# Kernel optimization log

Hardware: AMD Instinct MI355X
Metric: run time of the kernel (lower is better)

## Reference

```python
import jax, jax.numpy as jnp
import numpy as np
from jax import lax

H, W = 480, 320
BS, PAD, SF, WIN = 20, 6, 4, 32        # block, zero-pad, scale, window = BS+2*PAD
NH, NW = H // BS, W // BS              # 24, 16 -> 384 blocks


def _conv(x, w, b, stride=1, pad=0):
    out = lax.conv_general_dilated(x, w, (stride, stride), [(pad, pad), (pad, pad)],
                                   dimension_numbers=('NCHW', 'OIHW', 'NCHW'))
    return out + b[None, :, None, None]


def _rep_conv(x, w, b):  # 3x3 conv with replicate padding (padding_mode='replicate')
    xp = jnp.pad(x, ((0, 0), (0, 0), (1, 1), (1, 1)), mode='edge')
    return _conv(xp, w, b)


def _maxpool2(x):
    return lax.reduce_window(x, -jnp.inf, lax.max, (1, 1, 2, 2), (1, 1, 2, 2), 'VALID')


def _pixel_shuffle(x, r=SF):  # (N, C*r*r, h, w) -> (N, C, h*r, w*r), torch ordering
    n, crr, h, w = x.shape
    c = crr // (r * r)
    return x.reshape(n, c, r, r, h, w).transpose(0, 1, 4, 2, 5, 3).reshape(n, c, h * r, w * r)


def _he(key, shape):
    std = np.sqrt(2.0 / (shape[0] * shape[2] * shape[3]))
    return jax.random.normal(key, shape, jnp.float32) * std


def setup_inputs() -> dict:
    key = jax.random.key(0)
    ks = jax.random.split(key, 16)
    return {
        'x': jax.random.normal(ks[0], (1, 3, H, W), jnp.float32),
        'cls_w1': _he(ks[1], (32, 3, 3, 3)),  'cls_b1': jnp.zeros((32,), jnp.float32),
        'cls_w2': _he(ks[2], (32, 32, 3, 3)), 'cls_b2': jnp.zeros((32,), jnp.float32),
        'cls_w3': _he(ks[3], (16, 32, 3, 3)), 'cls_b3': jnp.zeros((16,), jnp.float32),
        'cls_w4': _he(ks[4], (8, 16, 3, 3)),  'cls_b4': jnp.zeros((8,), jnp.float32),
        'cls_w5': _he(ks[5], (1, 8, 5, 5)),   'cls_b5': jnp.zeros((1,), jnp.float32),
        'lt_w1': _he(ks[6], (16, 3, 3, 3)),   'lt_b1': jnp.zeros((16,), jnp.float32),
        'lt_w2': _he(ks[7], (48, 16, 3, 3)),  'lt_b2': jnp.zeros((48,), jnp.float32),
        'cx_w1': _he(ks[8], (64, 3, 3, 3)),   'cx_b1': jnp.zeros((64,), jnp.float32),
        'cx_w2': _he(ks[9], (64, 64, 3, 3)),  'cx_b2': jnp.zeros((64,), jnp.float32),
        'cx_w3': _he(ks[10], (48, 64, 3, 3)), 'cx_b3': jnp.zeros((48,), jnp.float32),
    }


def reference(x, cls_w1, cls_b1, cls_w2, cls_b2, cls_w3, cls_b3, cls_w4, cls_b4,
              cls_w5, cls_b5, lt_w1, lt_b1, lt_w2, lt_b2,
              cx_w1, cx_b1, cx_w2, cx_b2, cx_w3, cx_b3):
    relu = jax.nn.relu
    # ---- classifier (gate) ----
    h = relu(_rep_conv(x, cls_w1, cls_b1))
    h = _maxpool2(relu(_rep_conv(h, cls_w2, cls_b2)))
    h = relu(_rep_conv(h, cls_w3, cls_b3))
    h = _maxpool2(relu(_rep_conv(h, cls_w4, cls_b4)))
    h = _conv(h, cls_w5, cls_b5, stride=BS // 4)          # (1,1,NH,NW)
    class_vector = jax.nn.sigmoid(h.reshape(-1))          # (NH*NW,)

    # ---- blockify (overlapping 32x32 windows, stride 20, zero pad 6) ----
    xp = jnp.pad(x, ((0, 0), (0, 0), (PAD, PAD), (PAD, PAD)))
    hidx = jnp.arange(NH)[:, None] * BS + jnp.arange(WIN)
    widx = jnp.arange(NW)[:, None] * BS + jnp.arange(WIN)
    t = xp[:, :, hidx]
    t = t[:, :, :, :, widx]
    blocks = t.transpose(0, 2, 4, 1, 3, 5).reshape(NH * NW, 3, WIN, WIN)

    # ---- experts (run on all blocks; mask-select == one-hot gather/scatter) ----
    lt = _pixel_shuffle(_conv(relu(_conv(blocks, lt_w1, lt_b1, pad=1)), lt_w2, lt_b2, pad=1))
    lt = jnp.clip(lt, 0.0, 1.0)
    cx = relu(_conv(blocks, cx_w1, cx_b1, pad=1))
    cx = relu(_conv(cx, cx_w2, cx_b2, pad=1))
    cx = jnp.clip(_pixel_shuffle(_conv(cx, cx_w3, cx_b3, pad=1)), 0.0, 1.0)

    is_complex = class_vector > 0.5
    out = jnp.where(is_complex[:, None, None, None], cx, lt)  # (N,3,128,128)

    # ---- crop halo and reassemble full image ----
    c0 = SF * PAD
    out = out[:, :, c0:c0 + SF * BS, c0:c0 + SF * BS]          # (N,3,80,80)
    img = out.reshape(NH, NW, 3, SF * BS, SF * BS)
    img = img.transpose(2, 0, 3, 1, 4).reshape(1, 3, NH * SF * BS, NW * SF * BS)
    return img, class_vector
```

## Files before the change

### kernel.cpp

```cpp
#include <hip/hip_runtime.h>
#include <hip/hip_bf16.h>
#include <math.h>

static constexpr int H = 480, W = 320, NH = 24, NW = 16, NB = 384;
static constexpr int HW = H * W;
static constexpr int H2 = 240, W2 = 160;
static constexpr int HW2 = H2 * W2;
static constexpr int H4 = 120, W4 = 80;
static constexpr int HW4 = H4 * W4;
static constexpr int IMG_PIX = 3 * 1920 * 1280;

typedef __attribute__((ext_vector_type(8))) short short8;
typedef __attribute__((ext_vector_type(4))) float f32x4;
typedef __attribute__((ext_vector_type(8))) unsigned short ushort8;

static constexpr int WQ_CX2 = 0;
static constexpr int WQ_CX3 = 36864;
static constexpr int WQ_LT2 = 64512;
static constexpr int WQ_FCX = 78336;
static constexpr int WQ_FLT = 80384;
static constexpr int WQ_CLS2 = 80896;
static constexpr int WPK_ALL = 108544;

__device__ __forceinline__ int iclamp(int v, int lo, int hi) {
    return v < lo ? lo : (v > hi ? hi : v);
}
__device__ __forceinline__ unsigned short f2bfu(float x) {
    __hip_bfloat16 h = __float2bfloat16(x);
    return *reinterpret_cast<unsigned short*>(&h);
}
__device__ __forceinline__ float bf2f(unsigned short u) {
    __hip_bfloat16 h = *reinterpret_cast<__hip_bfloat16*>(&u);
    return __bfloat162float(h);
}

__global__ __launch_bounds__(256) void k_prep(const float* __restrict__ x,
                                              const float* __restrict__ cls_w1,
                                              const float* __restrict__ cls_b1,
                                              const float* __restrict__ cx_w2,
                                              const float* __restrict__ cx_w3,
                                              const float* __restrict__ lt_w2,
                                              const float* __restrict__ cx_w1,
                                              const float* __restrict__ lt_w1,
                                              const float* __restrict__ cls_w2,
                                              unsigned short* __restrict__ c1s,
                                              unsigned short* __restrict__ wpk) {
    int blk = blockIdx.x;
    if (blk < 2400) {
        int coc = blk / 600;
        int p = (blk - coc * 600) * 256 + threadIdx.x;
        if (p >= HW) return;
        int y = p / W, xx = p - y * W;
        float in[27];
#pragma unroll
        for (int ci = 0; ci < 3; ++ci)
#pragma unroll
            for (int dy = 0; dy < 3; ++dy) {
                int yy = iclamp(y + dy - 1, 0, H - 1);
#pragma unroll
                for (int dx = 0; dx < 3; ++dx) {
                    int xc = iclamp(xx + dx - 1, 0, W - 1);
                    in[ci * 9 + dy * 3 + dx] = x[ci * HW + yy * W + xc];
                }
            }
        ushort8 hv, mv, lv;
#pragma unroll
        for (int c8 = 0; c8 < 8; ++c8) {
            int co = coc * 8 + c8;
            float acc = cls_b1[co];
#pragma unroll
            for (int k = 0; k < 27; ++k) acc = fmaf(cls_w1[co * 27 + k], in[k], acc);
            float v = fmaxf(acc, 0.f);
            unsigned short h = f2bfu(v);
            float r1 = v - bf2f(h);
            unsigned short m = f2bfu(r1);
            unsigned short l = f2bfu(r1 - bf2f(m));
            hv[c8] = h; mv[c8] = m; lv[c8] = l;
        }
        *(ushort8*)(c1s + (long)p * 32 + coc * 8) = hv;
        *(ushort8*)(c1s + (long)32 * HW + (long)p * 32 + coc * 8) = mv;
        *(ushort8*)(c1s + (long)64 * HW + (long)p * 32 + coc * 8) = lv;
        return;
    }
    int i = (blk - 2400) * 256 + threadIdx.x;
    if (i >= WPK_ALL) return;
    float v = 0.f;
    if (i < WQ_CX3) {
        int c = i >> 9, r = i & 511;
        int lane = r >> 3, j = r & 7;
        int col = lane & 15, kq = lane >> 4;
        int nt = c & 3, kc = (c >> 2) & 1, t = c >> 3;
        int co = nt * 16 + col, ci = kc * 32 + kq * 8 + j;
        v = cx_w2[(co * 64 + ci) * 9 + t];
    } else if (i < WQ_LT2) {
        int c = (i - WQ_CX3) >> 9, r = i & 511;
        int lane = r >> 3, j = r & 7;
        int col = lane & 15, kq = lane >> 4;
        int nt = c % 3, q = c / 3;
        int kc = q & 1, t = q >> 1;
        int co = nt * 16 + col, ci = kc * 32 + kq * 8 + j;
        v = cx_w3[(co * 64 + ci) * 9 + t];
    } else if (i < WQ_FCX) {
        int c = (i - WQ_LT2) >> 9, r = i & 511;
        int lane = r >> 3, j = r & 7;
        int col = lane & 15, kq = lane >> 4;
        int nt = c % 3, t = c / 3;
        int co = nt * 16 + col, ci = kq * 8 + j;
        v = (ci < 16) ? lt_w2[(co * 16 + ci) * 9 + t] : 0.f;
    } else if (i < WQ_FLT) {
        int c = (i - WQ_FCX) >> 9, r = i & 511;
        int lane = r >> 3, j = r & 7;
        int col = lane & 15, kq = lane >> 4;
        int co = c * 16 + col, k = kq * 8 + j;
        v = (k < 27) ? cx_w1[co * 27 + k] : 0.f;
    } else if (i < WQ_CLS2) {
        int r = i & 511;
        int lane = r >> 3, j = r & 7;
        int col = lane & 15, kq = lane >> 4;
        int k = kq * 8 + j;
        v = (k < 27) ? lt_w1[col * 27 + k] : 0.f;
    } else {
        int c = (i - WQ_CLS2) >> 9, r = i & 511;
        int lane = r >> 3, j = r & 7;
        int col = lane & 15, kq = lane >> 4;
        int nt = c & 1, q = c >> 1;
        int t = q % 9, pl = q / 9;
        int co = nt * 16 + col, ci = kq * 8 + j;
        float w = cls_w2[(co * 32 + ci) * 9 + t];
        unsigned short h = f2bfu(w);
        float r1 = w - bf2f(h);
        unsigned short m = f2bfu(r1);
        unsigned short l = f2bfu(r1 - bf2f(m));
        wpk[i] = pl == 0 ? h : (pl == 1 ? m : l);
        return;
    }
    wpk[i] = f2bfu(v);
}


template <int P>
__device__ __forceinline__ void cls2_phase(const unsigned short* __restrict__ src,
                                           unsigned short* __restrict__ sh2,
                                           const unsigned short* __restrict__ wb,
                                           f32x4 acc[4][2], int tid, int ty, int tx) {
    int lane = tid & 63, wave = tid >> 6;
    int col = lane & 15, kq = lane >> 4;
    __syncthreads();
    for (int idx = tid; idx < 1296; idx += 256) {
        int pix = idx >> 2, g = idx & 3;
        int hy = iclamp(ty * 16 + pix / 18 - 1, 0, H - 1);
        int hx = iclamp(tx * 16 + pix % 18 - 1, 0, W - 1);
        ushort8 v = *(const ushort8*)(src + ((long)(hy * W + hx)) * 32 + g * 8);
        *(ushort8*)(sh2 + pix * 32 + ((g ^ ((pix >> 1) & 3)) * 8)) = v;
    }
    __syncthreads();
#pragma unroll
    for (int t = 0; t < 9; ++t) {
        int dy = t / 3, dx = t - dy * 3;
        short8 B[2][P];
#pragma unroll
        for (int nt = 0; nt < 2; ++nt)
#pragma unroll
            for (int pl = 0; pl < P; ++pl)
                B[nt][pl] = *(const short8*)(wb + ((pl * 9 + t) * 2 + nt) * 512 + lane * 8);
#pragma unroll
        for (int i = 0; i < 4; ++i) {
            int pix = (wave * 4 + i + dy) * 18 + col + dx;
            short8 a = *(const short8*)(sh2 + pix * 32 + ((kq ^ ((pix >> 1) & 3)) * 8));
#pragma unroll
            for (int nt = 0; nt < 2; ++nt)
#pragma unroll
                for (int pl = 0; pl < P; ++pl)
                    acc[i][nt] = __builtin_amdgcn_mfma_f32_16x16x32_bf16(a, B[nt][pl],
                                                                         acc[i][nt], 0, 0, 0);
        }
    }
}

__global__ __launch_bounds__(256, 2) void k_cls2m(const unsigned short* __restrict__ c1s,
                                                  const unsigned short* __restrict__ wpk,
                                                  const float* __restrict__ b2,
                                                  float* __restrict__ c2) {
    extern __shared__ unsigned short sh2[];
    int tid = threadIdx.x;
    int tile = blockIdx.x;
    int ty = tile / 20, tx = tile - ty * 20;
    int lane = tid & 63, wave = tid >> 6;
    int col = lane & 15, kq = lane >> 4;
    const unsigned short* wb = wpk + WQ_CLS2;
    f32x4 acc[4][2];
#pragma unroll
    for (int nt = 0; nt < 2; ++nt) {
        float bv = b2[nt * 16 + col];
#pragma unroll
        for (int i = 0; i < 4; ++i) acc[i][nt] = f32x4{bv, bv, bv, bv};
    }
    cls2_phase<3>(c1s, sh2, wb, acc, tid, ty, tx);
    cls2_phase<2>(c1s + (long)32 * HW, sh2, wb + 18 * 512, acc, tid, ty, tx);
    cls2_phase<1>(c1s + (long)64 * HW, sh2, wb + 36 * 512, acc, tid, ty, tx);
    __syncthreads();
    float* pool = (float*)sh2;
#pragma unroll
    for (int i = 0; i < 4; ++i)
#pragma unroll
        for (int nt = 0; nt < 2; ++nt)
#pragma unroll
            for (int rr = 0; rr < 4; ++rr)
                pool[(nt * 16 + col) * 257 + (wave * 4 + i) * 16 + kq * 4 + rr] =
                    fmaxf(acc[i][nt][rr], 0.f);
    __syncthreads();
#pragma unroll
    for (int k = 0; k < 8; ++k) {
        int o = tid + k * 256;
        int co = o >> 6, rem = o & 63;
        int py = rem >> 3, px = rem & 7;
        const float* lp = pool + co * 257 + py * 32 + px * 2;
        float m = fmaxf(fmaxf(lp[0], lp[1]), fmaxf(lp[16], lp[17]));
        c2[co * HW2 + (ty * 8 + py) * W2 + tx * 8 + px] = m;
    }
}

__global__ __launch_bounds__(256) void k_cls3(const float* __restrict__ in,
                                              const float* __restrict__ w,
                                              const float* __restrict__ b,
                                              float* __restrict__ p3) {
    int p = blockIdx.x * 256 + threadIdx.x;
    if (p >= HW2) return;
    int cc = blockIdx.y;
    int s = blockIdx.z;
    int y = p / W2, xx = p - y * W2;
    float acc[8];
#pragma unroll
    for (int co = 0; co < 8; ++co) acc[co] = s ? 0.f : b[cc * 8 + co];
    for (int cil = 0; cil < 16; ++cil) {
        int ci = s * 16 + cil;
        float v[9];
#pragma unroll
        for (int dy = 0; dy < 3; ++dy) {
            int yy = iclamp(y + dy - 1, 0, H2 - 1);
#pragma unroll
            for (int dx = 0; dx < 3; ++dx) {
                int xc = iclamp(xx + dx - 1, 0, W2 - 1);
                v[dy * 3 + dx] = in[ci * HW2 + yy * W2 + xc];
            }
        }
#pragma unroll
        for (int co = 0; co < 8; ++co)
#pragma unroll
            for (int k = 0; k < 9; ++k)
                acc[co] = fmaf(w[(cc * 8 + co) * 288 + ci * 9 + k], v[k], acc[co]);
    }
#pragma unroll
    for (int co = 0; co < 8; ++co) p3[(s * 16 + cc * 8 + co) * HW2 + p] = acc[co];
}

__global__ __launch_bounds__(256) void k_cls4f(const float* __restrict__ p3,
                                               const float* __restrict__ w,
                                               const float* __restrict__ b,
                                               float* __restrict__ out) {
    __shared__ float lds[8 * 256];
    int t = threadIdx.x;
    int tile = blockIdx.x;
    int ty = tile / 10, tx = tile - ty * 10;
    int ly = t >> 4, lx = t & 15;
    int y = ty * 16 + ly, xx = tx * 16 + lx;
    float acc[8];
#pragma unroll
    for (int co = 0; co < 8; ++co) acc[co] = b[co];
    for (int ci = 0; ci < 16; ++ci) {
        float v[9];
#pragma unroll
        for (int dy = 0; dy < 3; ++dy) {
            int yy = iclamp(y + dy - 1, 0, H2 - 1);
#pragma unroll
            for (int dx = 0; dx < 3; ++dx) {
                int xc = iclamp(xx + dx - 1, 0, W2 - 1);
                int idx = ci * HW2 + yy * W2 + xc;
                v[dy * 3 + dx] = fmaxf(p3[idx] + p3[idx + 16 * HW2], 0.f);
            }
        }
#pragma unroll
        for (int co = 0; co < 8; ++co) {
            const float* wp = w + co * 144 + ci * 9;
#pragma unroll
            for (int k = 0; k < 9; ++k) acc[co] = fmaf(wp[k], v[k], acc[co]);
        }
    }
#pragma unroll
    for (int co = 0; co < 8; ++co) lds[co * 256 + t] = fmaxf(acc[co], 0.f);
    __syncthreads();
#pragma unroll
    for (int k = 0; k < 2; ++k) {
        int o = t + k * 256;
        int co = o >> 6, rem = o & 63;
        int py = rem >> 3, px = rem & 7;
        const float* lp = lds + co * 256 + py * 32 + px * 2;
        float m = fmaxf(fmaxf(lp[0], lp[1]), fmaxf(lp[16], lp[17]));
        out[co * HW4 + (ty * 8 + py) * W4 + tx * 8 + px] = m;
    }
}

__global__ __launch_bounds__(64) void k_cls5(const float* __restrict__ in,
                                             const float* __restrict__ w,
                                             const float* __restrict__ b,
                                             float* __restrict__ clsv,
                                             float* __restrict__ out_cls) {
    int bidx = blockIdx.x;
    int oy = bidx / NW, ox = bidx - oy * NW;
    int lane = threadIdx.x;
    float s = 0.f;
    for (int k = lane; k < 200; k += 64) {
        int ci = k / 25, r = k - ci * 25;
        int ky = r / 5, kx = r - ky * 5;
        s = fmaf(w[k], in[ci * HW4 + (oy * 5 + ky) * W4 + (ox * 5 + kx)], s);
    }
#pragma unroll
    for (int off = 32; off; off >>= 1) s += __shfl_down(s, off, 64);
    if (lane == 0) {
        float sig = 1.f / (1.f + expf(-(s + b[0])));
        clsv[bidx] = sig;
        out_cls[bidx] = sig;
    }
}

__global__ __launch_bounds__(512)
__attribute__((amdgpu_waves_per_eu(4, 4)))
void k_block(const float* __restrict__ x,
             const unsigned short* __restrict__ wpk,
             const float* __restrict__ lt_b1,
             const float* __restrict__ cx_b1,
             const float* __restrict__ lt_b2,
             const float* __restrict__ cx_b2,
             const float* __restrict__ cx_b3,
             const float* __restrict__ clsv,
             float* __restrict__ out) {
    extern __shared__ unsigned short sh[];
    unsigned short* T1 = sh;
    unsigned short* T2 = sh + 16384;
    unsigned short* XH = sh + 28672;
    int wg = blockIdx.x;
    int b = wg / 5, e = wg - b * 5;
    bool cx = clsv[b] > 0.5f;
    int bh = b / NW, bw = b - bh * NW;
    int base = 6 + 4 * e;
    int tid = threadIdx.x;
    int lane = tid & 63, wave = tid >> 6;
    int col = lane & 15, kq = lane >> 4;

    if (!cx) {
        ushort8 z = {0, 0, 0, 0, 0, 0, 0, 0};
        for (int i = tid; i < 1024; i += 512) *(ushort8*)(T1 + i * 8) = z;
    }
    if (tid < 340) {
        int xr = tid / 34, xcc = tid - xr * 34;
        int yg = bh * 20 + (base - 3 + xr) - 6;
        int xg = bw * 20 + (xcc - 1) - 6;
        bool ok = (unsigned)yg < (unsigned)H && (unsigned)xg < (unsigned)W;
#pragma unroll
        for (int ci = 0; ci < 3; ++ci)
            XH[ci * 340 + tid] = ok ? f2bfu(x[ci * HW + yg * W + xg])
                                    : (unsigned short)0;
    }
    __syncthreads();

    if (cx) {
        short8 Bf[4];
        float bv[4];
#pragma unroll
        for (int nt = 0; nt < 4; ++nt) {
            Bf[nt] = *(const short8*)(wpk + WQ_FCX + nt * 512 + lane * 8);
            bv[nt] = cx_b1[nt * 16 + col];
        }
#pragma unroll
        for (int i = 0; i < 2; ++i) {
            int mt = wave + 8 * i;
            int tr = mt >> 1, xc0 = (mt & 1) << 4;
            short8 av;
#pragma unroll
            for (int j = 0; j < 8; ++j) {
                int k = kq * 8 + j;
                int kk = k < 27 ? k : 0;
                int ci = kk / 9, t = kk - ci * 9;
                int dy = t / 3, dx = t - dy * 3;
                unsigned short v = XH[ci * 340 + (tr + dy) * 34 + (xc0 + col + dx)];
                av[j] = (k < 27) ? (short)v : (short)0;
            }
#pragma unroll
            for (int nt = 0; nt < 4; ++nt) {
                f32x4 acc = {bv[nt], bv[nt], bv[nt], bv[nt]};
                acc = __builtin_amdgcn_mfma_f32_16x16x32_bf16(av, Bf[nt], acc, 0, 0, 0);
                int co = nt * 16 + col;
#pragma unroll
                for (int r = 0; r < 4; ++r) {
                    int p1 = mt * 16 + kq * 4 + r;
                    T1[p1 * 64 + (((co >> 3) ^ (p1 & 7)) << 3) + (co & 7)] =
                        f2bfu(fmaxf(acc[r], 0.f));
                }
            }
        }
    } else {
        short8 Bf = *(const short8*)(wpk + WQ_FLT + lane * 8);
        float bv = lt_b1[col];
#pragma unroll
        for (int i = 0; i < 2; ++i) {
            int mt = wave + 8 * i;
            int tr = mt >> 1, xc0 = (mt & 1) << 4;
            short8 av;
#pragma unroll
            for (int j = 0; j < 8; ++j) {
                int k = kq * 8 + j;
                int kk = k < 27 ? k : 0;
                int ci = kk / 9, t = kk - ci * 9;
                int dy = t / 3, dx = t - dy * 3;
                unsigned short v = XH[ci * 340 + (tr + dy) * 34 + (xc0 + col + dx)];
                av[j] = (k < 27) ? (short)v : (short)0;
            }
            f32x4 acc = {bv, bv, bv, bv};
            acc = __builtin_amdgcn_mfma_f32_16x16x32_bf16(av, Bf, acc, 0, 0, 0);
#pragma unroll
            for (int r = 0; r < 4; ++r) {
                int p1 = mt * 16 + kq * 4 + r;
                T1[p1 * 32 + (((col >> 3) ^ ((p1 >> 1) & 3)) << 3) + (col & 7)] =
                    f2bfu(fmaxf(acc[r], 0.f));
            }
        }
    }
    __syncthreads();

    if (cx) {
        {
            f32x4 acc[2][4];
#pragma unroll
            for (int nt = 0; nt < 4; ++nt) {
                float bv = cx_b2[nt * 16 + col];
#pragma unroll
                for (int i = 0; i < 2; ++i) acc[i][nt] = f32x4{bv, bv, bv, bv};
            }
#pragma unroll
            for (int t = 0; t < 9; ++t) {
                int dy = t / 3, dx = t - dy * 3;
                short8 B[4][2];
#pragma unroll
                for (int nt = 0; nt < 4; ++nt)
#pragma unroll
                    for (int kc = 0; kc < 2; ++kc)
                        B[nt][kc] = *(const short8*)(wpk + WQ_CX2 +
                                                     ((t * 2 + kc) * 4 + nt) * 512 +
                                                     lane * 8);
#pragma unroll
                for (int i = 0; i < 2; ++i) {
                    int mt = wave + 8 * i;
                    if (mt >= 12) continue;
                    int tr = (mt >> 1) + dy;
                    int xs = ((mt & 1) << 4) + col + dx - 1;
                    bool xv = (unsigned)xs < 32u;
                    int xcl = xs < 0 ? 0 : (xs > 31 ? 31 : xs);
                    int p1 = tr * 32 + xcl;
#pragma unroll
                    for (int kc = 0; kc < 2; ++kc) {
                        int c = kc * 4 + kq;
                        short8 a = *(const short8*)(T1 + p1 * 64 + ((c ^ (p1 & 7)) << 3));
                        if (!xv) a = short8{0, 0, 0, 0, 0, 0, 0, 0};
#pragma unroll
                        for (int nt = 0; nt < 4; ++nt)
                            acc[i][nt] = __builtin_amdgcn_mfma_f32_16x16x32_bf16(
                                a, B[nt][kc], acc[i][nt], 0, 0, 0);
                    }
                }
            }
#pragma unroll
            for (int i = 0; i < 2; ++i) {
                int mt = wave + 8 * i;
                if (mt >= 12) continue;
#pragma unroll
                for (int nt = 0; nt < 4; ++nt) {
                    int co = nt * 16 + col;
#pragma unroll
                    for (int r = 0; r < 4; ++r) {
                        int p2 = mt * 16 + kq * 4 + r;
                        T2[p2 * 64 + (((co >> 3) ^ (p2 & 7)) << 3) + (co & 7)] =
                            f2bfu(fmaxf(acc[i][nt][r], 0.f));
                    }
                }
            }
        }
        __syncthreads();
        {
            int mt = wave;
            f32x4 acc[3];
#pragma unroll
            for (int nt = 0; nt < 3; ++nt) {
                float bv = cx_b3[nt * 16 + col];
                acc[nt] = f32x4{bv, bv, bv, bv};
            }
#pragma unroll
            for (int t = 0; t < 9; ++t) {
                int dy = t / 3, dx = t - dy * 3;
                short8 B[3][2];
#pragma unroll
                for (int nt = 0; nt < 3; ++nt)
#pragma unroll
                    for (int kc = 0; kc < 2; ++kc)
                        B[nt][kc] = *(const short8*)(wpk + WQ_CX3 +
                                                     ((t * 2 + kc) * 3 + nt) * 512 +
                                                     lane * 8);
                int tr2 = (mt >> 1) + dy;
                int xs = ((mt & 1) << 4) + col + dx - 1;
                bool xv = (unsigned)xs < 32u;
                int xcl = xs < 0 ? 0 : (xs > 31 ? 31 : xs);
                int p2 = tr2 * 32 + xcl;
#pragma unroll
                for (int kc = 0; kc < 2; ++kc) {
                    int c = kc * 4 + kq;
                    short8 a = *(const short8*)(T2 + p2 * 64 + ((c ^ (p2 & 7)) << 3));
                    if (!xv) a = short8{0, 0, 0, 0, 0, 0, 0, 0};
#pragma unroll
                    for (int nt = 0; nt < 3; ++nt)
                        acc[nt] = __builtin_amdgcn_mfma_f32_16x16x32_bf16(
                            a, B[nt][kc], acc[nt], 0, 0, 0);
                }
            }
            int py = base + (mt >> 1);
#pragma unroll
            for (int nt = 0; nt < 3; ++nt) {
                int co = nt * 16 + col;
                int ch = co >> 4, dy2 = (co >> 2) & 3, dx2 = co & 3;
#pragma unroll
                for (int r = 0; r < 4; ++r) {
                    int p = mt * 16 + kq * 4 + r;
                    int px = p & 31;
                    int s0 = px * 4 + dx2 - 24;
                    if ((unsigned)s0 < 80u) {
                        int r0 = py * 4 + dy2 - 24;
                        float v = fminf(fmaxf(acc[nt][r], 0.f), 1.f);
                        out[ch * 2457600 + (bh * 80 + r0) * 1280 + bw * 80 + s0] = v;
                    }
                }
            }
        }
    } else {
        int mt = wave;
        f32x4 acc[3];
#pragma unroll
        for (int nt = 0; nt < 3; ++nt) {
            float bv = lt_b2[nt * 16 + col];
            acc[nt] = f32x4{bv, bv, bv, bv};
        }
#pragma unroll
        for (int t = 0; t < 9; ++t) {
            int dy = t / 3, dx = t - dy * 3;
            short8 B[3];
#pragma unroll
            for (int nt = 0; nt < 3; ++nt)
                B[nt] = *(const short8*)(wpk + WQ_LT2 + (t * 3 + nt) * 512 + lane * 8);
            int tr = (mt >> 1) + 1 + dy;
            int xs = ((mt & 1) << 4) + col + dx - 1;
            bool xv = (unsigned)xs < 32u;
            int xcl = xs < 0 ? 0 : (xs > 31 ? 31 : xs);
            int p1 = tr * 32 + xcl;
            short8 a = *(const short8*)(T1 + p1 * 32 + ((kq ^ ((p1 >> 1) & 3)) << 3));
            if (!xv) a = short8{0, 0, 0, 0, 0, 0, 0, 0};
#pragma unroll
            for (int nt = 0; nt < 3; ++nt)
                acc[nt] = __builtin_amdgcn_mfma_f32_16x16x32_bf16(a, B[nt], acc[nt], 0, 0, 0);
        }
        int py = base + (mt >> 1);
#pragma unroll
        for (int nt = 0; nt < 3; ++nt) {
            int co = nt * 16 + col;
            int ch = co >> 4, dy2 = (co >> 2) & 3, dx2 = co & 3;
#pragma unroll
            for (int r = 0; r < 4; ++r) {
                int p = mt * 16 + kq * 4 + r;
                int px = p & 31;
                int s0 = px * 4 + dx2 - 24;
                if ((unsigned)s0 < 80u) {
                    int r0 = py * 4 + dy2 - 24;
                    float v = fminf(fmaxf(acc[nt][r], 0.f), 1.f);
                    out[ch * 2457600 + (bh * 80 + r0) * 1280 + bw * 80 + s0] = v;
                }
            }
        }
    }
}

extern "C" void kernel_launch(void* const* d_in, const int* in_sizes, int n_in,
                              void* d_out, int out_size, void* d_ws, size_t ws_size,
                              hipStream_t stream) {
    const float* x      = (const float*)d_in[0];
    const float* cls_w1 = (const float*)d_in[1];
    const float* cls_b1 = (const float*)d_in[2];
    const float* cls_w2 = (const float*)d_in[3];
    const float* cls_b2 = (const float*)d_in[4];
    const float* cls_w3 = (const float*)d_in[5];
    const float* cls_b3 = (const float*)d_in[6];
    const float* cls_w4 = (const float*)d_in[7];
    const float* cls_b4 = (const float*)d_in[8];
    const float* cls_w5 = (const float*)d_in[9];
    const float* cls_b5 = (const float*)d_in[10];
    const float* lt_w1  = (const float*)d_in[11];
    const float* lt_b1  = (const float*)d_in[12];
    const float* lt_w2  = (const float*)d_in[13];
    const float* lt_b2  = (const float*)d_in[14];
    const float* cx_w1  = (const float*)d_in[15];
    const float* cx_b1  = (const float*)d_in[16];
    const float* cx_w2  = (const float*)d_in[17];
    const float* cx_b2  = (const float*)d_in[18];
    const float* cx_w3  = (const float*)d_in[19];
    const float* cx_b3  = (const float*)d_in[20];

    float* ws = (float*)d_ws;
    float* out = (float*)d_out;

    size_t off = 0;
    float* c2 = ws + off;   off += (size_t)32 * HW2;
    float* c4 = ws + off;   off += (size_t)8 * HW4;
    float* clsv = ws + off; off += 384;
    unsigned short* wpk = (unsigned short*)(ws + off); off += (WPK_ALL + 1) / 2;
    size_t fixed = off;

    unsigned short* c1s = (unsigned short*)(ws + fixed);
    float* p3 = ws + fixed + (size_t)48 * HW;

    (void)hipFuncSetAttribute((const void*)k_cls2m,
                              hipFuncAttributeMaxDynamicSharedMemorySize, 32896);
    (void)hipFuncSetAttribute((const void*)k_block,
                              hipFuncAttributeMaxDynamicSharedMemorySize, 59384);

    k_prep<<<2400 + (WPK_ALL + 255) / 256, 256, 0, stream>>>(
        x, cls_w1, cls_b1, cx_w2, cx_w3, lt_w2, cx_w1, lt_w1, cls_w2, c1s, wpk);
    k_cls2m<<<600, 256, 32896, stream>>>(c1s, wpk, cls_b2, c2);
    k_cls3<<<dim3(150, 2, 2), 256, 0, stream>>>(c2, cls_w3, cls_b3, p3);
    k_cls4f<<<150, 256, 0, stream>>>(p3, cls_w4, cls_b4, c4);
    k_cls5<<<NB, 64, 0, stream>>>(c4, cls_w5, cls_b5, clsv, out + IMG_PIX);
    k_block<<<NB * 5, 512, 59384, stream>>>(x, wpk, lt_b1, cx_b1, lt_b2, cx_b2,
                                            cx_b3, clsv, out);
}
```

Measured before the change: 169.5 us.

## Double-buffer conv weight taps through LDS with prefetch in k_block

Weights for each 3x3 tap of the cx2, cx3 and lt2 convolutions are now staged into a double-buffered LDS region. The next tap is prefetched from global memory into registers while the MFMAs for the current tap run. This replaces the per-wave global loads of B fragments with LDS reads, aiming to hide global latency. It adds a __syncthreads per tap and raises the dynamic LDS size per workgroup, which may limit occupancy.

```diff
diff --git a/kernel.cpp b/kernel.cpp
--- a/kernel.cpp
+++ b/kernel.cpp
@@ -338,6 +338,7 @@
     unsigned short* T1 = sh;
     unsigned short* T2 = sh + 16384;
     unsigned short* XH = sh + 28672;
+    unsigned short* WB = sh + 29696;
     int wg = blockIdx.x;
     int b = wg / 5, e = wg - b * 5;
     bool cx = clsv[b] > 0.5f;
@@ -398,6 +399,10 @@
                 }
             }
         }
+        {
+            ushort8 nb0 = *(const ushort8*)(wpk + WQ_CX2 + tid * 8);
+            *(ushort8*)(WB + tid * 8) = nb0;
+        }
     } else {
         short8 Bf = *(const short8*)(wpk + WQ_FLT + lane * 8);
         float bv = lt_b1[col];
@@ -424,6 +429,10 @@
                     f2bfu(fmaxf(acc[r], 0.f));
             }
         }
+        if (tid < 192) {
+            ushort8 nb0 = *(const ushort8*)(wpk + WQ_LT2 + tid * 8);
+            *(ushort8*)(WB + tid * 8) = nb0;
+        }
     }
     __syncthreads();
 
@@ -439,14 +448,16 @@
 #pragma unroll
             for (int t = 0; t < 9; ++t) {
                 int dy = t / 3, dx = t - dy * 3;
+                ushort8 nb;
+                if (t < 8)
+                    nb = *(const ushort8*)(wpk + WQ_CX2 + (t + 1) * 4096 + tid * 8);
+                const unsigned short* WBc = WB + (t & 1) * 4096;
                 short8 B[4][2];
 #pragma unroll
                 for (int nt = 0; nt < 4; ++nt)
 #pragma unroll
                     for (int kc = 0; kc < 2; ++kc)
-                        B[nt][kc] = *(const short8*)(wpk + WQ_CX2 +
-                                                     ((t * 2 + kc) * 4 + nt) * 512 +
-                                                     lane * 8);
+                        B[nt][kc] = *(const short8*)(WBc + (kc * 4 + nt) * 512 + lane * 8);
 #pragma unroll
                 for (int i = 0; i < 2; ++i) {
                     int mt = wave + 8 * i;
@@ -467,6 +478,9 @@
                                 a, B[nt][kc], acc[i][nt], 0, 0, 0);
                     }
                 }
+                if (t < 8)
+                    *(ushort8*)(WB + ((t + 1) & 1) * 4096 + tid * 8) = nb;
+                __syncthreads();
             }
 #pragma unroll
             for (int i = 0; i < 2; ++i) {
@@ -483,6 +497,10 @@
                     }
                 }
             }
+            if (tid < 384) {
+                ushort8 nb0 = *(const ushort8*)(wpk + WQ_CX3 + tid * 8);
+                *(ushort8*)(WB + tid * 8) = nb0;
+            }
         }
         __syncthreads();
         {
@@ -496,14 +514,16 @@
 #pragma unroll
             for (int t = 0; t < 9; ++t) {
                 int dy = t / 3, dx = t - dy * 3;
+                ushort8 nb;
+                if (t < 8 && tid < 384)
+                    nb = *(const ushort8*)(wpk + WQ_CX3 + (t + 1) * 3072 + tid * 8);
+                const unsigned short* WBc = WB + (t & 1) * 4096;
                 short8 B[3][2];
 #pragma unroll
                 for (int nt = 0; nt < 3; ++nt)
 #pragma unroll
                     for (int kc = 0; kc < 2; ++kc)
-                        B[nt][kc] = *(const short8*)(wpk + WQ_CX3 +
-                                                     ((t * 2 + kc) * 3 + nt) * 512 +
-                                                     lane * 8);
+                        B[nt][kc] = *(const short8*)(WBc + (kc * 3 + nt) * 512 + lane * 8);
                 int tr2 = (mt >> 1) + dy;
                 int xs = ((mt & 1) << 4) + col + dx - 1;
                 bool xv = (unsigned)xs < 32u;
@@ -518,6 +538,11 @@
                     for (int nt = 0; nt < 3; ++nt)
                         acc[nt] = __builtin_amdgcn_mfma_f32_16x16x32_bf16(
                             a, B[nt][kc], acc[nt], 0, 0, 0);
+                }
+                if (t < 8) {
+                    if (tid < 384)
+                        *(ushort8*)(WB + ((t + 1) & 1) * 4096 + tid * 8) = nb;
+                    __syncthreads();
                 }
             }
             int py = base + (mt >> 1);
@@ -549,10 +574,14 @@
 #pragma unroll
         for (int t = 0; t < 9; ++t) {
             int dy = t / 3, dx = t - dy * 3;
+            ushort8 nb;
+            if (t < 8 && tid < 192)
+                nb = *(const ushort8*)(wpk + WQ_LT2 + (t + 1) * 1536 + tid * 8);
+            const unsigned short* WBc = WB + (t & 1) * 4096;
             short8 B[3];
 #pragma unroll
             for (int nt = 0; nt < 3; ++nt)
-                B[nt] = *(const short8*)(wpk + WQ_LT2 + (t * 3 + nt) * 512 + lane * 8);
+                B[nt] = *(const short8*)(WBc + nt * 512 + lane * 8);
             int tr = (mt >> 1) + 1 + dy;
             int xs = ((mt & 1) << 4) + col + dx - 1;
             bool xv = (unsigned)xs < 32u;
@@ -563,6 +592,11 @@
 #pragma unroll
             for (int nt = 0; nt < 3; ++nt)
                 acc[nt] = __builtin_amdgcn_mfma_f32_16x16x32_bf16(a, B[nt], acc[nt], 0, 0, 0);
+            if (t < 8) {
+                if (tid < 192)
+                    *(ushort8*)(WB + ((t + 1) & 1) * 4096 + tid * 8) = nb;
+                __syncthreads();
+            }
         }
         int py = base + (mt >> 1);
 #pragma unroll
@@ -625,7 +659,7 @@
     (void)hipFuncSetAttribute((const void*)k_cls2m,
                               hipFuncAttributeMaxDynamicSharedMemorySize, 32896);
     (void)hipFuncSetAttribute((const void*)k_block,
-                              hipFuncAttributeMaxDynamicSharedMemorySize, 59384);
+                              hipFuncAttributeMaxDynamicSharedMemorySize, 75776);
 
     k_prep<<<2400 + (WPK_ALL + 255) / 256, 256, 0, stream>>>(
         x, cls_w1, cls_b1, cx_w2, cx_w3, lt_w2, cx_w1, lt_w1, cls_w2, c1s, wpk);
@@ -633,6 +667,6 @@
     k_cls3<<<dim3(150, 2, 2), 256, 0, stream>>>(c2, cls_w3, cls_b3, p3);
     k_cls4f<<<150, 256, 0, stream>>>(p3, cls_w4, cls_b4, c4);
     k_cls5<<<NB, 64, 0, stream>>>(c4, cls_w5, cls_b5, clsv, out + IMG_PIX);
-    k_block<<<NB * 5, 512, 59384, stream>>>(x, wpk, lt_b1, cx_b1, lt_b2, cx_b2,
+    k_block<<<NB * 5, 512, 75776, stream>>>(x, wpk, lt_b1, cx_b1, lt_b2, cx_b2,
                                             cx_b3, clsv, out);
 }
```

Measured after the change: 153.8 us, median of 2. 1.1x faster.
